# Kernel tuning notes

Measured on AMD Instinct MI355X. Metric: run time of the kernel, lower is better.

## Reference

```python
import jax, jax.numpy as jnp
import numpy as np
from jax import lax


def setup_inputs() -> dict:
    key = jax.random.key(0)
    k1, k2 = jax.random.split(key)
    x = jax.random.normal(k1, (16, 256, 128, 128), dtype=jnp.float32)
    # Conv2d(2, 1, 7, padding=3, bias=False) weight, PyTorch layout [out, in, kH, kW]
    w = jax.random.normal(k2, (1, 2, 7, 7), dtype=jnp.float32) * (1.0 / np.sqrt(2 * 7 * 7))
    return {"x": x, "w": w}


def reference(x, w):
    # Channel-wise mean and max, keepdim -> [B,1,H,W] each, concat -> [B,2,H,W]
    avg_out = jnp.mean(x, axis=1, keepdims=True)
    max_out = jnp.max(x, axis=1, keepdims=True)
    s = jnp.concatenate([avg_out, max_out], axis=1)
    # Redundant FFT2 -> IFFT2 round trip (identity up to numerics), faithful to source
    s = jnp.fft.ifft2(jnp.fft.fft2(s)).real.astype(x.dtype)
    # 2->1 channel 'same' conv (cross-correlation, matching torch Conv2d), padding=3
    out = lax.conv_general_dilated(
        s, w,
        window_strides=(1, 1),
        padding=((3, 3), (3, 3)),
        dimension_numbers=("NCHW", "OIHW", "NCHW"),
    )
    return jax.nn.sigmoid(out)
```

## Files before the change

kernel.cpp:

```cpp
#include <hip/hip_runtime.h>
#include <math.h>


#define BB 16
#define CC 256
#define HH 128
#define WW 128
#define HW (HH * WW)
#define CHW (CC * HW)
#define HW4 (HW / 4)
#define NPOS (BB * HW)
#define NG (BB * HW4)

typedef float floatx4 __attribute__((ext_vector_type(4)));

__global__ __launch_bounds__(512) void reduce_mean_max_kernel(
    const float* __restrict__ x, float* __restrict__ s) {
  const int tid  = threadIdx.x;
  const int lane = tid & 63;
  const int q    = tid >> 6;
  const int g    = blockIdx.x * 64 + lane;
  const int b    = g >> 12;
  const int off  = g & 4095;

  const floatx4* p =
      (const floatx4*)(x + (size_t)b * CHW) + off + (size_t)(q * 32) * HW4;

  floatx4 sum = (floatx4)(0.f);
  floatx4 mx  = (floatx4)(-INFINITY);

#pragma unroll 8
  for (int i = 0; i < 32; ++i) {
    floatx4 v = __builtin_nontemporal_load(p + (size_t)i * HW4);
    sum += v;
    mx.x = fmaxf(mx.x, v.x); mx.y = fmaxf(mx.y, v.y);
    mx.z = fmaxf(mx.z, v.z); mx.w = fmaxf(mx.w, v.w);
  }

  __shared__ floatx4 s_sum[8][64];
  __shared__ floatx4 s_max[8][64];
  s_sum[q][lane] = sum;
  s_max[q][lane] = mx;
  __syncthreads();

  if (tid < 64) {
    floatx4 ts = s_sum[0][tid];
    floatx4 tm = s_max[0][tid];
#pragma unroll
    for (int qq = 1; qq < 8; ++qq) {
      floatx4 a = s_sum[qq][tid];
      floatx4 m = s_max[qq][tid];
      ts += a;
      tm.x = fmaxf(tm.x, m.x); tm.y = fmaxf(tm.y, m.y);
      tm.z = fmaxf(tm.z, m.z); tm.w = fmaxf(tm.w, m.w);
    }
    ts *= (1.0f / (float)CC);

    floatx4* outa = (floatx4*)(s + (size_t)b * 2 * HW) + off;
    floatx4* outm = (floatx4*)(s + (size_t)b * 2 * HW + HW) + off;
    *outa = ts;
    *outm = tm;
  }
}

__global__ __launch_bounds__(256) void conv_sigmoid_kernel(
    const float* __restrict__ s, const float* __restrict__ w,
    float* __restrict__ out) {
  __shared__ float wf[2 * 49];
  const int tid = threadIdx.x;
  if (tid < 2 * 49) wf[tid] = w[tid];
  __syncthreads();

  const int idx = blockIdx.x * 256 + tid;
  const int b   = idx >> 14;
  const int hw  = idx & 16383;
  const int y   = hw >> 7;
  const int xpo = hw & 127;

  const float* sb = s + (size_t)b * 2 * HW;

  float acc = 0.0f;
#pragma unroll
  for (int ci = 0; ci < 2; ++ci) {
    const float* sc = sb + ci * HW;
    const float* wc = wf + ci * 49;
#pragma unroll
    for (int kh = 0; kh < 7; ++kh) {
      const int yy = y + kh - 3;
      if (yy < 0 || yy >= HH) continue;
      const float* row = sc + yy * WW;
#pragma unroll
      for (int kw = 0; kw < 7; ++kw) {
        const int xx = xpo + kw - 3;
        if (xx < 0 || xx >= WW) continue;
        acc = fmaf(row[xx], wc[kh * 7 + kw], acc);
      }
    }
  }

  out[idx] = 1.0f / (1.0f + expf(-acc));
}

extern "C" void kernel_launch(void* const* d_in, const int* in_sizes, int n_in,
                              void* d_out, int out_size, void* d_ws, size_t ws_size,
                              hipStream_t stream) {
  const float* x = (const float*)d_in[0];
  const float* w = (const float*)d_in[1];
  float* out = (float*)d_out;
  float* s   = (float*)d_ws;

  reduce_mean_max_kernel<<<NG / 64, 512, 0, stream>>>(x, s);

  conv_sigmoid_kernel<<<NPOS / 256, 256, 0, stream>>>(s, w, out);
}
```

Baseline: 360.8 us.

## Tile conv input in shared memory with register row reuse; split reduce epilogue

The conv kernel now stages a padded 14-row band of both pooled channels in shared memory. Each thread computes four vertically adjacent outputs, reusing loaded column values across kernel rows, and boundary checks are removed via zero padding. The reduce kernel's final combine is split so one wavefront handles the mean and another the max. This cuts redundant global/L2 loads in the conv, at the cost of fewer blocks (256) and lower parallelism.

```diff
diff --git a/kernel.cpp b/kernel.cpp
--- a/kernel.cpp
+++ b/kernel.cpp
@@ -43,62 +43,92 @@
   s_max[q][lane] = mx;
   __syncthreads();
 
-  if (tid < 64) {
-    floatx4 ts = s_sum[0][tid];
-    floatx4 tm = s_max[0][tid];
+  if (tid < 128) {
+    const int l   = tid & 63;
+    const int gg  = blockIdx.x * 64 + l;
+    const int bb  = gg >> 12;
+    const int of2 = gg & 4095;
+    if (tid < 64) {
+      floatx4 ts = s_sum[0][l];
 #pragma unroll
-    for (int qq = 1; qq < 8; ++qq) {
-      floatx4 a = s_sum[qq][tid];
-      floatx4 m = s_max[qq][tid];
-      ts += a;
-      tm.x = fmaxf(tm.x, m.x); tm.y = fmaxf(tm.y, m.y);
-      tm.z = fmaxf(tm.z, m.z); tm.w = fmaxf(tm.w, m.w);
+      for (int qq = 1; qq < 8; ++qq) ts += s_sum[qq][l];
+      ts *= (1.0f / (float)CC);
+      ((floatx4*)(s + (size_t)bb * 2 * HW))[of2] = ts;
+    } else {
+      floatx4 tm = s_max[0][l];
+#pragma unroll
+      for (int qq = 1; qq < 8; ++qq) {
+        floatx4 m = s_max[qq][l];
+        tm.x = fmaxf(tm.x, m.x); tm.y = fmaxf(tm.y, m.y);
+        tm.z = fmaxf(tm.z, m.z); tm.w = fmaxf(tm.w, m.w);
+      }
+      ((floatx4*)(s + (size_t)bb * 2 * HW + HW))[of2] = tm;
     }
-    ts *= (1.0f / (float)CC);
-
-    floatx4* outa = (floatx4*)(s + (size_t)b * 2 * HW) + off;
-    floatx4* outm = (floatx4*)(s + (size_t)b * 2 * HW + HW) + off;
-    *outa = ts;
-    *outm = tm;
   }
 }
+
+#define BAND 8
+#define TR   14
+#define LDW  136
 
 __global__ __launch_bounds__(256) void conv_sigmoid_kernel(
     const float* __restrict__ s, const float* __restrict__ w,
     float* __restrict__ out) {
+  __shared__ float tile[2][TR][LDW];
   __shared__ float wf[2 * 49];
-  const int tid = threadIdx.x;
+
+  const int tid  = threadIdx.x;
+  const int blk  = blockIdx.x;
+  const int b    = blk >> 4;
+  const int band = blk & 15;
+  const int y0   = band * BAND;
+
   if (tid < 2 * 49) wf[tid] = w[tid];
+
+  const int grp = tid >> 5;
+  const int l32 = tid & 31;
+  for (int job = grp; job < 2 * TR; job += 8) {
+    const int ci = (job >= TR) ? 1 : 0;
+    const int r  = ci ? (job - TR) : job;
+    const int yy = y0 + r - 3;
+    const bool inrow = (yy >= 0 && yy < HH);
+    const float* src = s + ((size_t)b * 2 + ci) * HW + (size_t)yy * WW;
+    float* dst = tile[ci][r];
+    for (int c = l32; c < LDW; c += 32) {
+      const int xx = c - 3;
+      dst[c] = (inrow && xx >= 0 && xx < WW) ? src[xx] : 0.f;
+    }
+  }
   __syncthreads();
 
-  const int idx = blockIdx.x * 256 + tid;
-  const int b   = idx >> 14;
-  const int hw  = idx & 16383;
-  const int y   = hw >> 7;
-  const int xpo = hw & 127;
+  const int xpo  = tid & 127;
+  const int ysub = (tid >> 7) * 4;
 
-  const float* sb = s + (size_t)b * 2 * HW;
-
-  float acc = 0.0f;
+  float acc0 = 0.f, acc1 = 0.f, acc2 = 0.f, acc3 = 0.f;
 #pragma unroll
   for (int ci = 0; ci < 2; ++ci) {
-    const float* sc = sb + ci * HW;
-    const float* wc = wf + ci * 49;
 #pragma unroll
-    for (int kh = 0; kh < 7; ++kh) {
-      const int yy = y + kh - 3;
-      if (yy < 0 || yy >= HH) continue;
-      const float* row = sc + yy * WW;
+    for (int kw = 0; kw < 7; ++kw) {
+      float v[10];
 #pragma unroll
-      for (int kw = 0; kw < 7; ++kw) {
-        const int xx = xpo + kw - 3;
-        if (xx < 0 || xx >= WW) continue;
-        acc = fmaf(row[xx], wc[kh * 7 + kw], acc);
+      for (int r = 0; r < 10; ++r) v[r] = tile[ci][ysub + r][xpo + kw];
+      const float* wc = wf + ci * 49 + kw;
+#pragma unroll
+      for (int kh = 0; kh < 7; ++kh) {
+        const float wv = wc[kh * 7];
+        acc0 = fmaf(v[kh],     wv, acc0);
+        acc1 = fmaf(v[kh + 1], wv, acc1);
+        acc2 = fmaf(v[kh + 2], wv, acc2);
+        acc3 = fmaf(v[kh + 3], wv, acc3);
       }
     }
   }
 
-  out[idx] = 1.0f / (1.0f + expf(-acc));
+  float* ob = out + (size_t)b * HW + (size_t)(y0 + ysub) * WW + xpo;
+  ob[0]      = 1.0f / (1.0f + expf(-acc0));
+  ob[WW]     = 1.0f / (1.0f + expf(-acc1));
+  ob[2 * WW] = 1.0f / (1.0f + expf(-acc2));
+  ob[3 * WW] = 1.0f / (1.0f + expf(-acc3));
 }
 
 extern "C" void kernel_launch(void* const* d_in, const int* in_sizes, int n_in,
@@ -111,5 +141,5 @@
 
   reduce_mean_max_kernel<<<NG / 64, 512, 0, stream>>>(x, s);
 
-  conv_sigmoid_kernel<<<NPOS / 256, 256, 0, stream>>>(s, w, out);
+  conv_sigmoid_kernel<<<BB * (HH / BAND), 256, 0, stream>>>(s, w, out);
 }
```

After: 351.7 us. 2.5% less time.
